# Performance work log

Hardware: AMD Instinct MI355X
Metric: run time of the kernel (lower is better)

Reference implementation:

```python
import jax, jax.numpy as jnp
import numpy as np

KERNEL_SIZE = 11
PAD = KERNEL_SIZE // 2
SIGMA = (KERNEL_SIZE - 1) * 2.0  # default sigma in the torch module


def _gaussian_kernel(ks, sigma):
    x = np.arange(ks, dtype=np.float32)
    g = np.exp(-(x - ks // 2) ** 2 / (2.0 * sigma ** 2))
    g = g / g.sum()
    k2d = np.outer(g, g).astype(np.float32)
    return jnp.asarray(k2d)[None, None]  # [1,1,ks,ks]


def setup_inputs() -> dict:
    key = jax.random.key(0)
    k1, k2 = jax.random.split(key)
    B, C, H, W = 16, 1, 1024, 1024
    img1 = jax.random.uniform(k1, (B, C, H, W), dtype=jnp.float32)
    img2 = jax.random.uniform(k2, (B, C, H, W), dtype=jnp.float32)
    kernel = _gaussian_kernel(KERNEL_SIZE, SIGMA)
    return {"img1": img1, "img2": img2, "kernel": kernel}


def _conv(x, kernel):
    # single-channel conv2d, 'same' padding (pad = k//2)
    return jax.lax.conv_general_dilated(
        x, kernel, window_strides=(1, 1),
        padding=[(PAD, PAD), (PAD, PAD)],
        dimension_numbers=("NCHW", "OIHW", "NCHW"))


def reference(img1, img2, kernel):
    val_range = (jnp.maximum(img1.max(), img2.max())
                 - jnp.minimum(img1.min(), img2.min()) + 1e-5)
    mu1 = _conv(img1, kernel)
    mu2 = _conv(img2, kernel)
    d1 = img1 - mu1
    d2 = img2 - mu2
    sigma1_sq = _conv(d1 * d1, kernel) + 1.0
    sigma2_sq = _conv(d2 * d2, kernel) + 1.0
    sigma12 = _conv(d1 * d2, kernel) + 1.0
    mu1_sq = mu1 * mu1 + 1.0
    mu2_sq = mu2 * mu2 + 1.0
    mu1mu2 = mu1 * mu2 + 1.0
    C1 = (0.01 * val_range) ** 2
    C2 = (0.03 * val_range) ** 2
    structure = (2.0 * sigma12 + C2) / (sigma1_sq + sigma2_sq + C2)
    brightness = ((2.0 * mu1mu2) ** 2 + C1) / ((mu1_sq + mu2_sq) ** 2 + C1)
    ssim_map = structure * brightness  # valid_mask=None -> all-ones mask
    return 1.0 - ssim_map.mean()
```

## Files before the change

### kernel.cpp

```cpp
#include <hip/hip_runtime.h>
#include <hip/hip_fp16.h>


#define IMG_H 1024
#define IMG_W 1024
#define USEC   44
#define NSTRIP 24
#define BAND   64
#define NBAND  16
#define NBATCH 16
#define NWAVES (NSTRIP * NBAND * NBATCH)
#define NBLK   (NWAVES / 4)

__device__ __forceinline__ unsigned fkey(float f) {
  unsigned b = __float_as_uint(f);
  return (b & 0x80000000u) ? ~b : (b | 0x80000000u);
}
__device__ __forceinline__ float funkey(unsigned k) {
  return (k & 0x80000000u) ? __uint_as_float(k & 0x7FFFFFFFu)
                           : __uint_as_float(~k);
}

__device__ __forceinline__ unsigned xlane_u(unsigned v, int addr) {
  return (unsigned)__builtin_amdgcn_ds_bpermute(addr, (int)v);
}

__global__ void ssim_init(unsigned* __restrict__ ws) {
  ws[0] = 0u;
  ws[1] = 0u;
  ws[2] = 0u;
  ws[3] = 0xFFFFFFFFu;
  ws[4] = 0u;
  ws[5] = 0u;
}

__global__ __launch_bounds__(256, 2)
void ssim_main(const float* __restrict__ img1, const float* __restrict__ img2,
               const float* __restrict__ kern, unsigned* __restrict__ ws,
               float* __restrict__ out) {
  __shared__ float redbuf[4][8];

  const int tid = threadIdx.x;
  const int lane = tid & 63;
  const int wv = tid >> 6;
  const int wid = blockIdx.x * 4 + wv;

  const int strip = wid % NSTRIP;
  const int rem = wid / NSTRIP;
  const int band = rem % NBAND;
  const int batch = rem / NBAND;

  const size_t boff = (size_t)batch * (IMG_H * IMG_W);
  const float* i1 = img1 + boff;
  const float* i2 = img2 + boff;

  float g[11];
  #pragma unroll
  for (int j = 0; j < 11; ++j) {
    float gv = kern[55 + j] * rsqrtf(kern[60]);
    g[j] = __uint_as_float(
        (unsigned)__builtin_amdgcn_readfirstlane(__float_as_uint(gv)));
  }

  const int col = strip * USEC + lane - 10;
  const bool cok = (col >= 0) && (col < IMG_W);
  const int cidx = min(max(col, 0), IMG_W - 1);
  const bool oma = (lane >= 10) && (lane < 54) && (col < IMG_W);
  const int r0 = band * BAND;
  const int a4 = lane * 4;

  float w1[11] = {}, w2[11] = {};
  float m1w[11] = {}, m2w[11] = {};
  float p11[11] = {}, p22[11] = {}, p12[11] = {};

  float acc0 = 0.f, aC1 = 0.f, aC2 = 0.f;
  float vmin = 1e30f, vmax = -1e30f;

  float nv1, nv2;
  {
    int rin = r0 - 10;
    if ((unsigned)rin < IMG_H) {
      nv1 = i1[(size_t)rin * IMG_W + cidx];
      nv2 = i2[(size_t)rin * IMG_W + cidx];
    } else { nv1 = 0.f; nv2 = 0.f; }
  }

  #pragma unroll 1
  for (int m = 0; m < 8; ++m) {
    #pragma unroll
    for (int c = 0; c < 11; ++c) {
      const int t = m * 11 + c;

      float v1 = cok ? nv1 : 0.f;
      float v2 = cok ? nv2 : 0.f;
      w1[c] = v1; w2[c] = v2;
      vmin = fminf(vmin, fminf(v1, v2));
      vmax = fmaxf(vmax, fmaxf(v1, v2));

      if (t < 83) {
        int rin = r0 - 9 + t;
        if ((unsigned)rin < IMG_H) {
          nv1 = i1[(size_t)rin * IMG_W + cidx];
          nv2 = i2[(size_t)rin * IMG_W + cidx];
        } else { nv1 = 0.f; nv2 = 0.f; }
      } else { nv1 = 0.f; nv2 = 0.f; }

      float V1 = 0.f, V2 = 0.f;
      #pragma unroll
      for (int j = 0; j < 11; ++j) {
        V1 = fmaf(g[j], w1[(c + 1 + j) % 11], V1);
        V2 = fmaf(g[j], w2[(c + 1 + j) % 11], V2);
      }

      unsigned pv;
      {
        __half2 pV = __floats2half2_rn(V1, V2);
        pv = *(unsigned*)&pV;
      }
      float mu1 = g[5] * V1, mu2 = g[5] * V2;
      #pragma unroll
      for (int o = 1; o <= 5; ++o) {
        unsigned ul = xlane_u(pv, a4 - 4 * o);
        unsigned ur = xlane_u(pv, a4 + 4 * o);
        __half2 hl = *(__half2*)&ul;
        __half2 hr = *(__half2*)&ur;
        float sg = g[5 + o];
        mu1 = fmaf(sg, __low2float(hl), mu1);
        mu1 = fmaf(sg, __low2float(hr), mu1);
        mu2 = fmaf(sg, __high2float(hl), mu2);
        mu2 = fmaf(sg, __high2float(hr), mu2);
      }
      m1w[c] = mu1; m2w[c] = mu2;

      const bool drok = ((unsigned)(r0 - 15 + t) < IMG_H);
      float d1 = (drok && cok) ? (w1[(c + 6) % 11] - mu1) : 0.f;
      float d2 = (drok && cok) ? (w2[(c + 6) % 11] - mu2) : 0.f;

      unsigned pd;
      {
        __half2 pD = __floats2half2_rn(d1, d2);
        pd = *(unsigned*)&pD;
      }
      float h11 = (g[5] * d1) * d1;
      float h22 = (g[5] * d2) * d2;
      float h12 = (g[5] * d1) * d2;
      #pragma unroll
      for (int o = 1; o <= 5; ++o) {
        unsigned ul = xlane_u(pd, a4 - 4 * o);
        unsigned ur = xlane_u(pd, a4 + 4 * o);
        __half2 hl = *(__half2*)&ul;
        __half2 hr = *(__half2*)&ur;
        float l1 = __low2float(hl), l2 = __high2float(hl);
        float r1 = __low2float(hr), r2 = __high2float(hr);
        float u = g[5 + o];
        h11 = fmaf(u, fmaf(l1, l1, r1 * r1), h11);
        h22 = fmaf(u, fmaf(l2, l2, r2 * r2), h22);
        h12 = fmaf(u, fmaf(l1, l2, r1 * r2), h12);
      }
      p11[c] = h11; p22[c] = h22; p12[c] = h12;

      if (t >= 20 && t < 84) {
        float s11 = 0.f, s22 = 0.f, s12 = 0.f;
        #pragma unroll
        for (int j = 0; j < 11; ++j) {
          float gj = g[j];
          s11 = fmaf(gj, p11[(c + 1 + j) % 11], s11);
          s22 = fmaf(gj, p22[(c + 1 + j) % 11], s22);
          s12 = fmaf(gj, p12[(c + 1 + j) % 11], s12);
        }
        float M1 = m1w[(c + 6) % 11], M2 = m2w[(c + 6) % 11];

        float s1 = s11 + 1.f;
        float s2 = s22 + 1.f;
        float sv = s12 + 1.f;
        float a = 2.f * sv;
        float b = s1 + s2;
        float rb = __builtin_amdgcn_rcpf(b);
        float S0 = a * rb;
        float Sp = (b - a) * rb * rb;
        float m12 = fmaf(M1, M2, 1.f);
        float nb = 2.f * m12;
        float N1 = nb * nb;
        float ms = fmaf(M1, M1, fmaf(M2, M2, 2.f));
        float Dv = ms * ms;
        float rD = __builtin_amdgcn_rcpf(Dv);
        float B0 = N1 * rD;
        float Bp = (Dv - N1) * rD * rD;
        float t0v = S0 * B0, t1v = S0 * Bp, t2v = B0 * Sp;
        acc0 += oma ? t0v : 0.f;
        aC1 += oma ? t1v : 0.f;
        aC2 += oma ? t2v : 0.f;
      }
    }
  }

  #pragma unroll
  for (int off = 32; off > 0; off >>= 1) {
    acc0 += __shfl_down(acc0, off);
    aC1 += __shfl_down(aC1, off);
    aC2 += __shfl_down(aC2, off);
    vmin = fminf(vmin, __shfl_down(vmin, off));
    vmax = fmaxf(vmax, __shfl_down(vmax, off));
  }
  if (lane == 0) {
    redbuf[wv][0] = acc0; redbuf[wv][1] = aC1; redbuf[wv][2] = aC2;
    redbuf[wv][3] = vmin; redbuf[wv][4] = vmax;
  }
  __syncthreads();
  if (tid == 0) {
    float t0 = 0.f, t1 = 0.f, t2 = 0.f, mn = 1e30f, mx = -1e30f;
    #pragma unroll
    for (int w2 = 0; w2 < 4; ++w2) {
      t0 += redbuf[w2][0]; t1 += redbuf[w2][1]; t2 += redbuf[w2][2];
      mn = fminf(mn, redbuf[w2][3]); mx = fmaxf(mx, redbuf[w2][4]);
    }
    float* wsF = (float*)ws;
    atomicAdd(&wsF[0], t0);
    atomicAdd(&wsF[1], t1);
    atomicAdd(&wsF[2], t2);
    atomicMin(&ws[3], fkey(mn));
    atomicMax(&ws[4], fkey(mx));

    __threadfence();
    unsigned done = atomicAdd(&ws[5], 1u);
    if (done == gridDim.x - 1) {
      float s0 = atomicAdd(&wsF[0], 0.f);
      float sc1 = atomicAdd(&wsF[1], 0.f);
      float sc2 = atomicAdd(&wsF[2], 0.f);
      unsigned mnk = atomicMin(&ws[3], 0xFFFFFFFFu);
      unsigned mxk = atomicMax(&ws[4], 0u);
      float vr = funkey(mxk) - funkey(mnk) + 1e-5f;
      float c1 = 0.01f * vr; c1 *= c1;
      float c2 = 0.03f * vr; c2 *= c2;
      float mean = (s0 + c1 * sc1 + c2 * sc2) * (1.0f / 16777216.0f);
      out[0] = 1.f - mean;
    }
  }
}

extern "C" void kernel_launch(void* const* d_in, const int* in_sizes, int n_in,
                              void* d_out, int out_size, void* d_ws, size_t ws_size,
                              hipStream_t stream) {
  const float* img1 = (const float*)d_in[0];
  const float* img2 = (const float*)d_in[1];
  const float* kern = (const float*)d_in[2];
  unsigned* ws = (unsigned*)d_ws;
  float* out = (float*)d_out;
  (void)in_sizes; (void)n_in; (void)out_size; (void)ws_size;

  hipLaunchKernelGGL(ssim_init, dim3(1), dim3(1), 0, stream, ws);
  hipLaunchKernelGGL(ssim_main, dim3(NBLK), dim3(256), 0, stream,
                     img1, img2, kern, ws, out);
}
```

Before: 345.8 us.

## Software-pipeline vertical pass and cross-lane permutes one row ahead

Restructures the per-row loop so the next row's vertical conv and its ds_bpermute exchanges are issued before the current row's variance stage consumes its own permuted values. This hides LDS-permute latency behind independent ALU work. Launch bounds drop from two blocks to one per CU to give the compiler more registers for the extra in-flight values. The readfirstlane scalarisation of the Gaussian weights is also removed. The cost is lower occupancy and more live registers.

```diff
diff --git a/kernel.cpp b/kernel.cpp
--- a/kernel.cpp
+++ b/kernel.cpp
@@ -20,10 +20,11 @@
   return (k & 0x80000000u) ? __uint_as_float(k & 0x7FFFFFFFu)
                            : __uint_as_float(~k);
 }
-
 __device__ __forceinline__ unsigned xlane_u(unsigned v, int addr) {
   return (unsigned)__builtin_amdgcn_ds_bpermute(addr, (int)v);
 }
+__device__ __forceinline__ __half2 u2h(unsigned u) { return *(__half2*)&u; }
+__device__ __forceinline__ unsigned h2u(__half2 h) { return *(unsigned*)&h; }
 
 __global__ void ssim_init(unsigned* __restrict__ ws) {
   ws[0] = 0u;
@@ -34,7 +35,7 @@
   ws[5] = 0u;
 }
 
-__global__ __launch_bounds__(256, 2)
+__global__ __launch_bounds__(256, 1)
 void ssim_main(const float* __restrict__ img1, const float* __restrict__ img2,
                const float* __restrict__ kern, unsigned* __restrict__ ws,
                float* __restrict__ out) {
@@ -56,11 +57,7 @@
 
   float g[11];
   #pragma unroll
-  for (int j = 0; j < 11; ++j) {
-    float gv = kern[55 + j] * rsqrtf(kern[60]);
-    g[j] = __uint_as_float(
-        (unsigned)__builtin_amdgcn_readfirstlane(__float_as_uint(gv)));
-  }
+  for (int j = 0; j < 11; ++j) g[j] = kern[55 + j] * rsqrtf(kern[60]);
 
   const int col = strip * USEC + lane - 10;
   const bool cok = (col >= 0) && (col < IMG_W);
@@ -73,123 +70,160 @@
   float m1w[11] = {}, m2w[11] = {};
   float p11[11] = {}, p22[11] = {}, p12[11] = {};
 
+  unsigned vxl[5], vxr[5];
+  float V1c, V2c;
+  float nv1, nv2;
+
   float acc0 = 0.f, aC1 = 0.f, aC2 = 0.f;
   float vmin = 1e30f, vmax = -1e30f;
 
-  float nv1, nv2;
   {
     int rin = r0 - 10;
+    float a1 = 0.f, a2 = 0.f;
+    if ((unsigned)rin < IMG_H) {
+      a1 = i1[(size_t)rin * IMG_W + cidx];
+      a2 = i2[(size_t)rin * IMG_W + cidx];
+    }
+    float v1 = cok ? a1 : 0.f;
+    float v2 = cok ? a2 : 0.f;
+    w1[0] = v1; w2[0] = v2;
+    vmin = fminf(vmin, fminf(v1, v2));
+    vmax = fmaxf(vmax, fmaxf(v1, v2));
+  }
+  {
+    int rin = r0 - 9;
     if ((unsigned)rin < IMG_H) {
       nv1 = i1[(size_t)rin * IMG_W + cidx];
       nv2 = i2[(size_t)rin * IMG_W + cidx];
     } else { nv1 = 0.f; nv2 = 0.f; }
   }
+  {
+    float V1 = 0.f, V2 = 0.f;
+    #pragma unroll
+    for (int j = 0; j < 11; ++j) {
+      int ix = (1 + j) % 11;
+      V1 = fmaf(g[j], w1[ix], V1);
+      V2 = fmaf(g[j], w2[ix], V2);
+    }
+    unsigned pv = h2u(__floats2half2_rn(V1, V2));
+    #pragma unroll
+    for (int o = 1; o <= 5; ++o) {
+      vxl[o - 1] = xlane_u(pv, a4 - 4 * o);
+      vxr[o - 1] = xlane_u(pv, a4 + 4 * o);
+    }
+    V1c = V1; V2c = V2;
+  }
 
   #pragma unroll 1
   for (int m = 0; m < 8; ++m) {
     #pragma unroll
     for (int c = 0; c < 11; ++c) {
       const int t = m * 11 + c;
-
-      float v1 = cok ? nv1 : 0.f;
-      float v2 = cok ? nv2 : 0.f;
-      w1[c] = v1; w2[c] = v2;
-      vmin = fminf(vmin, fminf(v1, v2));
-      vmax = fmaxf(vmax, fmaxf(v1, v2));
-
-      if (t < 83) {
-        int rin = r0 - 9 + t;
-        if ((unsigned)rin < IMG_H) {
-          nv1 = i1[(size_t)rin * IMG_W + cidx];
-          nv2 = i2[(size_t)rin * IMG_W + cidx];
-        } else { nv1 = 0.f; nv2 = 0.f; }
-      } else { nv1 = 0.f; nv2 = 0.f; }
-
-      float V1 = 0.f, V2 = 0.f;
-      #pragma unroll
-      for (int j = 0; j < 11; ++j) {
-        V1 = fmaf(g[j], w1[(c + 1 + j) % 11], V1);
-        V2 = fmaf(g[j], w2[(c + 1 + j) % 11], V2);
-      }
-
-      unsigned pv;
-      {
-        __half2 pV = __floats2half2_rn(V1, V2);
-        pv = *(unsigned*)&pV;
-      }
-      float mu1 = g[5] * V1, mu2 = g[5] * V2;
-      #pragma unroll
-      for (int o = 1; o <= 5; ++o) {
-        unsigned ul = xlane_u(pv, a4 - 4 * o);
-        unsigned ur = xlane_u(pv, a4 + 4 * o);
-        __half2 hl = *(__half2*)&ul;
-        __half2 hr = *(__half2*)&ur;
-        float sg = g[5 + o];
-        mu1 = fmaf(sg, __low2float(hl), mu1);
-        mu1 = fmaf(sg, __low2float(hr), mu1);
-        mu2 = fmaf(sg, __high2float(hl), mu2);
-        mu2 = fmaf(sg, __high2float(hr), mu2);
-      }
-      m1w[c] = mu1; m2w[c] = mu2;
-
-      const bool drok = ((unsigned)(r0 - 15 + t) < IMG_H);
-      float d1 = (drok && cok) ? (w1[(c + 6) % 11] - mu1) : 0.f;
-      float d2 = (drok && cok) ? (w2[(c + 6) % 11] - mu2) : 0.f;
-
-      unsigned pd;
-      {
-        __half2 pD = __floats2half2_rn(d1, d2);
-        pd = *(unsigned*)&pD;
-      }
-      float h11 = (g[5] * d1) * d1;
-      float h22 = (g[5] * d2) * d2;
-      float h12 = (g[5] * d1) * d2;
-      #pragma unroll
-      for (int o = 1; o <= 5; ++o) {
-        unsigned ul = xlane_u(pd, a4 - 4 * o);
-        unsigned ur = xlane_u(pd, a4 + 4 * o);
-        __half2 hl = *(__half2*)&ul;
-        __half2 hr = *(__half2*)&ur;
-        float l1 = __low2float(hl), l2 = __high2float(hl);
-        float r1 = __low2float(hr), r2 = __high2float(hr);
-        float u = g[5 + o];
-        h11 = fmaf(u, fmaf(l1, l1, r1 * r1), h11);
-        h22 = fmaf(u, fmaf(l2, l2, r2 * r2), h22);
-        h12 = fmaf(u, fmaf(l1, l2, r1 * r2), h12);
-      }
-      p11[c] = h11; p22[c] = h22; p12[c] = h12;
-
-      if (t >= 20 && t < 84) {
-        float s11 = 0.f, s22 = 0.f, s12 = 0.f;
+      if (t < 84) {
+        const int i6 = (c + 6) % 11;
+
+        float mu1 = g[5] * V1c, mu2 = g[5] * V2c;
         #pragma unroll
-        for (int j = 0; j < 11; ++j) {
-          float gj = g[j];
-          s11 = fmaf(gj, p11[(c + 1 + j) % 11], s11);
-          s22 = fmaf(gj, p22[(c + 1 + j) % 11], s22);
-          s12 = fmaf(gj, p12[(c + 1 + j) % 11], s12);
-        }
-        float M1 = m1w[(c + 6) % 11], M2 = m2w[(c + 6) % 11];
-
-        float s1 = s11 + 1.f;
-        float s2 = s22 + 1.f;
-        float sv = s12 + 1.f;
-        float a = 2.f * sv;
-        float b = s1 + s2;
-        float rb = __builtin_amdgcn_rcpf(b);
-        float S0 = a * rb;
-        float Sp = (b - a) * rb * rb;
-        float m12 = fmaf(M1, M2, 1.f);
-        float nb = 2.f * m12;
-        float N1 = nb * nb;
-        float ms = fmaf(M1, M1, fmaf(M2, M2, 2.f));
-        float Dv = ms * ms;
-        float rD = __builtin_amdgcn_rcpf(Dv);
-        float B0 = N1 * rD;
-        float Bp = (Dv - N1) * rD * rD;
-        float t0v = S0 * B0, t1v = S0 * Bp, t2v = B0 * Sp;
-        acc0 += oma ? t0v : 0.f;
-        aC1 += oma ? t1v : 0.f;
-        aC2 += oma ? t2v : 0.f;
+        for (int o = 1; o <= 5; ++o) {
+          __half2 hl = u2h(vxl[o - 1]);
+          __half2 hr = u2h(vxr[o - 1]);
+          float sg = g[5 + o];
+          mu1 = fmaf(sg, __low2float(hl), mu1);
+          mu1 = fmaf(sg, __low2float(hr), mu1);
+          mu2 = fmaf(sg, __high2float(hl), mu2);
+          mu2 = fmaf(sg, __high2float(hr), mu2);
+        }
+        m1w[c] = mu1; m2w[c] = mu2;
+
+        const bool drok = ((unsigned)(r0 - 15 + t) < IMG_H);
+        float d1 = (drok && cok) ? (w1[i6] - mu1) : 0.f;
+        float d2 = (drok && cok) ? (w2[i6] - mu2) : 0.f;
+        unsigned pd = h2u(__floats2half2_rn(d1, d2));
+        unsigned dxl[5], dxr[5];
+        #pragma unroll
+        for (int o = 1; o <= 5; ++o) {
+          dxl[o - 1] = xlane_u(pd, a4 - 4 * o);
+          dxr[o - 1] = xlane_u(pd, a4 + 4 * o);
+        }
+
+        if (t < 83) {
+          const int cn = (c + 1) % 11;
+          float v1 = cok ? nv1 : 0.f;
+          float v2 = cok ? nv2 : 0.f;
+          w1[cn] = v1; w2[cn] = v2;
+          vmin = fminf(vmin, fminf(v1, v2));
+          vmax = fmaxf(vmax, fmaxf(v1, v2));
+          if (t < 82) {
+            int rin = r0 - 8 + t;
+            if ((unsigned)rin < IMG_H) {
+              nv1 = i1[(size_t)rin * IMG_W + cidx];
+              nv2 = i2[(size_t)rin * IMG_W + cidx];
+            } else { nv1 = 0.f; nv2 = 0.f; }
+          }
+          float V1 = 0.f, V2 = 0.f;
+          #pragma unroll
+          for (int j = 0; j < 11; ++j) {
+            int ix = (cn + 1 + j) % 11;
+            V1 = fmaf(g[j], w1[ix], V1);
+            V2 = fmaf(g[j], w2[ix], V2);
+          }
+          unsigned pv = h2u(__floats2half2_rn(V1, V2));
+          #pragma unroll
+          for (int o = 1; o <= 5; ++o) {
+            vxl[o - 1] = xlane_u(pv, a4 - 4 * o);
+            vxr[o - 1] = xlane_u(pv, a4 + 4 * o);
+          }
+          V1c = V1; V2c = V2;
+        }
+
+        float h11 = (g[5] * d1) * d1;
+        float h22 = (g[5] * d2) * d2;
+        float h12 = (g[5] * d1) * d2;
+        #pragma unroll
+        for (int o = 1; o <= 5; ++o) {
+          __half2 hl = u2h(dxl[o - 1]);
+          __half2 hr = u2h(dxr[o - 1]);
+          float l1 = __low2float(hl), l2 = __high2float(hl);
+          float r1 = __low2float(hr), r2 = __high2float(hr);
+          float u = g[5 + o];
+          h11 = fmaf(u, fmaf(l1, l1, r1 * r1), h11);
+          h22 = fmaf(u, fmaf(l2, l2, r2 * r2), h22);
+          h12 = fmaf(u, fmaf(l1, l2, r1 * r2), h12);
+        }
+        p11[c] = h11; p22[c] = h22; p12[c] = h12;
+
+        if (t >= 20) {
+          float s11 = 0.f, s22 = 0.f, s12 = 0.f;
+          #pragma unroll
+          for (int j = 0; j < 11; ++j) {
+            float gj = g[j];
+            s11 = fmaf(gj, p11[(c + 1 + j) % 11], s11);
+            s22 = fmaf(gj, p22[(c + 1 + j) % 11], s22);
+            s12 = fmaf(gj, p12[(c + 1 + j) % 11], s12);
+          }
+          float M1 = m1w[i6], M2 = m2w[i6];
+
+          float s1 = s11 + 1.f;
+          float s2 = s22 + 1.f;
+          float sv = s12 + 1.f;
+          float a = 2.f * sv;
+          float b = s1 + s2;
+          float rb = __builtin_amdgcn_rcpf(b);
+          float S0 = a * rb;
+          float Sp = (b - a) * rb * rb;
+          float m12 = fmaf(M1, M2, 1.f);
+          float nb = 2.f * m12;
+          float N1 = nb * nb;
+          float ms = fmaf(M1, M1, fmaf(M2, M2, 2.f));
+          float Dv = ms * ms;
+          float rD = __builtin_amdgcn_rcpf(Dv);
+          float B0 = N1 * rD;
+          float Bp = (Dv - N1) * rD * rD;
+          float t0v = S0 * B0, t1v = S0 * Bp, t2v = B0 * Sp;
+          acc0 += oma ? t0v : 0.f;
+          aC1 += oma ? t1v : 0.f;
+          aC2 += oma ? t2v : 0.f;
+        }
       }
     }
   }
```

Result: slower. 378.4 us (+9.4%).
